# Kernel tuning notes

Hardware: AMD Instinct MI355X
Metric: run time of the kernel (lower is better)

## Reference

```python
import jax, jax.numpy as jnp
import numpy as np

B_SZ, C, H, W = 64, 256, 28, 28
HEADS, HEAD_DIM = 4, 64
BLOCK, HALO = 4, 4
WIN = BLOCK + 2 * HALO  # 12
KCONV = 3


def _unfold(x, k, s, p):
    # torch F.unfold semantics; returns [b, c, oh, kh, ow, kw]
    b, c, h, w = x.shape
    xp = jnp.pad(x, ((0, 0), (0, 0), (p, p), (p, p)))
    oh = (h + 2 * p - k) // s + 1
    ow = (w + 2 * p - k) // s + 1
    ih = jnp.arange(oh)[:, None] * s + jnp.arange(k)[None, :]
    iw = jnp.arange(ow)[:, None] * s + jnp.arange(k)[None, :]
    pt = xp[:, :, ih]            # [b,c,oh,kh,Wp]
    pt = pt[:, :, :, :, iw]      # [b,c,oh,kh,ow,kw]
    return pt


def _rel_to_abs(x):
    # x: [b, l, 2r-1] -> [b, l, r] via shift trick
    b, l, m = x.shape
    r = (m + 1) // 2
    x = jnp.pad(x, ((0, 0), (0, 0), (0, 1))).reshape(b, l * (m + 1))
    x = jnp.pad(x, ((0, 0), (0, m - l))).reshape(b, l + 1, m)
    return x[:, :l, -r:]


def _relative_logits_1d(q, rel_k):
    # q: [b, x, y, d], rel_k: [2r-1, d] -> [b, x, i(=r), y, j(=r)]
    b, h, w, _ = q.shape
    r = (rel_k.shape[0] + 1) // 2
    logits = jnp.einsum('bxyd,rd->bxyr', q, rel_k)
    logits = _rel_to_abs(logits.reshape(b * h, w, 2 * r - 1)).reshape(b, h, w, r)
    return jnp.broadcast_to(logits[:, :, None], (b, h, r, w, r))


def _rel_pos_emb(q, rel_height, rel_width):
    # q: [B, block^2, d]
    B, n, d = q.shape
    qb = q.reshape(B, BLOCK, BLOCK, d)
    lw = _relative_logits_1d(qb, rel_width)                 # [B,x,i,y,j]
    lw = lw.transpose(0, 1, 3, 2, 4).reshape(B, n, -1)      # b (x y) (i j)
    qh = qb.transpose(0, 2, 1, 3)
    lh = _relative_logits_1d(qh, rel_height)                # [B,y,i,x,j]
    lh = lh.transpose(0, 3, 1, 4, 2).reshape(B, n, -1)      # b (y x) (j i)
    return lw + lh


def setup_inputs() -> dict:
    key = jax.random.key(0)
    ks = jax.random.split(key, 13)
    f = jnp.float32
    rel_scale = HEAD_DIM ** (-0.5)
    return {
        'x': jax.random.normal(ks[0], (B_SZ, C, H, W), dtype=f),
        'w1': jax.random.normal(ks[1], (C, C), dtype=f) * 0.05,
        'b1': jax.random.normal(ks[2], (C,), dtype=f) * 0.05,
        'w2': jax.random.normal(ks[3], (C, C), dtype=f) * 0.05,
        'b2': jax.random.normal(ks[4], (C,), dtype=f) * 0.05,
        'w3': jax.random.normal(ks[5], (C, C), dtype=f) * 0.05,
        'b3': jax.random.normal(ks[6], (C,), dtype=f) * 0.05,
        'fc_w': jax.random.normal(ks[7], (KCONV * KCONV, 3 * HEADS), dtype=f) * 0.1,
        'dep_w': jax.random.normal(ks[8], (C, KCONV * KCONV, KCONV, KCONV), dtype=f) * 0.05,
        'rel_height': jax.random.normal(ks[9], (2 * WIN - 1, HEAD_DIM), dtype=f) * rel_scale,
        'rel_width': jax.random.normal(ks[10], (2 * WIN - 1, HEAD_DIM), dtype=f) * rel_scale,
        'rate1': jax.random.normal(ks[11], (1,), dtype=f),
        'rate2': jax.random.normal(ks[12], (1,), dtype=f),
    }


def reference(x, w1, b1, w2, b2, w3, b3, fc_w, dep_w, rel_height, rel_width, rate1, rate2):
    b = x.shape[0]
    scaling = HEAD_DIM ** (-0.5)
    q = jnp.einsum('bchw,oc->bohw', x, w1) + b1[None, :, None, None]
    k = jnp.einsum('bchw,oc->bohw', x, w2) + b2[None, :, None, None]
    v = jnp.einsum('bchw,oc->bohw', x, w3) + b3[None, :, None, None]
    c = q.shape[1]
    nb = H // BLOCK          # 7 blocks per side
    nwin = nb * nb           # 49 windows
    n_q = BLOCK * BLOCK      # 16 queries per window
    n_k = WIN * WIN          # 144 keys per window (with halo)

    # block queries: b c (h p1) (w p2) -> (b h w) (p1 p2) c
    q_att = q.reshape(b, c, nb, BLOCK, nb, BLOCK).transpose(0, 2, 4, 3, 5, 1).reshape(b * nwin, n_q, c)
    kp = _unfold(k, WIN, BLOCK, HALO).transpose(0, 2, 4, 3, 5, 1).reshape(b * nwin, n_k, c)
    vp = _unfold(v, WIN, BLOCK, HALO).transpose(0, 2, 4, 3, 5, 1).reshape(b * nwin, n_k, c)

    def split_heads(t):
        Bn, n, _ = t.shape
        return t.reshape(Bn, n, HEADS, HEAD_DIM).transpose(0, 2, 1, 3).reshape(Bn * HEADS, n, HEAD_DIM)

    q1 = split_heads(q_att) * scaling
    k1 = split_heads(kp)
    v1 = split_heads(vp)

    sim = jnp.einsum('bid,bjd->bij', q1, k1)
    sim = sim + _rel_pos_emb(q1, rel_height, rel_width)

    # NOTE: faithfully reproduces original (valid positions get -max, padded get 0)
    ones = jnp.ones((1, 1, H, W), x.dtype)
    valid = _unfold(ones, WIN, BLOCK, HALO).transpose(0, 2, 4, 3, 5, 1).reshape(nwin, n_k) > 0
    big_neg = -jnp.finfo(sim.dtype).max
    sim = sim.reshape(b, nwin, HEADS, n_q, n_k)
    sim = jnp.where(valid[None, :, None, None, :], big_neg, sim)
    attn = jax.nn.softmax(sim, axis=-1).reshape(b * nwin * HEADS, n_q, n_k)

    out = jnp.einsum('bij,bjd->bid', attn, v1)
    out = out.reshape(b * nwin, HEADS, n_q, HEAD_DIM).transpose(0, 2, 1, 3)  # merge heads
    out = out.reshape(b, nb, nb, BLOCK, BLOCK, c)
    out_att = out.transpose(0, 5, 1, 3, 2, 4).reshape(b, c, H, W)

    # conv branch: fc over concatenated per-head q,k,v, then depthwise-grouped conv
    f_all = jnp.concatenate([
        q.reshape(b, HEADS, HEAD_DIM, H * W),
        k.reshape(b, HEADS, HEAD_DIM, H * W),
        v.reshape(b, HEADS, HEAD_DIM, H * W)], axis=1)        # [b, 3*heads, hd, HW]
    f_all = jnp.einsum('bcmn,oc->bomn', f_all, fc_w)          # [b, 9, hd, HW]
    f_conv = f_all.transpose(0, 2, 1, 3).reshape(b, HEAD_DIM * KCONV * KCONV, H, W)
    out_conv = jax.lax.conv_general_dilated(
        f_conv, dep_w, window_strides=(1, 1), padding=((1, 1), (1, 1)),
        dimension_numbers=('NCHW', 'OIHW', 'NCHW'), feature_group_count=HEAD_DIM)

    return rate1[0] * out_att + rate2[0] * out_conv
```

## Files before the change

kernel.cpp:

```cpp
#include <hip/hip_runtime.h>
#include <hip/hip_bf16.h>

typedef __hip_bfloat16 bf16;
typedef unsigned int uint;
typedef unsigned short ushort;

using frag8 = __attribute__((ext_vector_type(8))) short;
using f32x4 = __attribute__((ext_vector_type(4))) float;

#define HWH 784
#define PPITCH 30
#define PPLANE 900
#define PBLK 10800

__global__ __launch_bounds__(256) void fold_w2(const float* __restrict__ fc_w,
                                               const float* __restrict__ dep_w,
                                               const float* __restrict__ b1,
                                               const float* __restrict__ b2,
                                               const float* __restrict__ b3,
                                               float* __restrict__ W2,
                                               float* __restrict__ biascat) {
    int idx = blockIdx.x * 256 + threadIdx.x;
    if (idx < 768) {
        const float* bs = idx < 256 ? b1 : (idx < 512 ? b2 : b3);
        biascat[idx] = bs[idx & 255];
    }
    if (idx >= 256 * 108) return;
    int oc  = idx / 108;
    int r   = idx % 108;
    int c12 = r / 9;
    int k9  = r % 9;
    float s = 0.f;
#pragma unroll
    for (int o = 0; o < 9; ++o)
        s += fc_w[o * 12 + c12] * dep_w[oc * 81 + o * 9 + k9];
    W2[idx] = s;
}

__global__ __launch_bounds__(256) void wprep(const float* __restrict__ w1,
                                             const float* __restrict__ w2,
                                             const float* __restrict__ w3,
                                             bf16* __restrict__ wbf) {
    int row = blockIdx.x, tid = threadIdx.x;
    const float* src = row < 256 ? w1 : (row < 512 ? w2 : w3);
    wbf[row * 256 + tid] = __float2bfloat16(src[(row & 255) * 256 + tid]);
}

__global__ __launch_bounds__(256) void xpose(const float* __restrict__ x,
                                             bf16* __restrict__ xT) {
    __shared__ float t[32][33];
    const int n0 = blockIdx.x * 32, c0 = blockIdx.y * 32, b = blockIdx.z;
    const int tid = threadIdx.x;
    const float* xb = x + (size_t)b * (256 * HWH);
#pragma unroll
    for (int e = tid; e < 1024; e += 256) {
        int r = e >> 5, col = e & 31;
        int n = n0 + col;
        t[r][col] = (n < HWH) ? xb[(size_t)(c0 + r) * HWH + n] : 0.f;
    }
    __syncthreads();
#pragma unroll
    for (int e = tid; e < 512; e += 256) {
        int r = e >> 4, cp = (e & 15) * 2;
        int n = n0 + r;
        if (n < HWH) {
            __hip_bfloat162 h;
            h.x = __float2bfloat16(t[cp][r]);
            h.y = __float2bfloat16(t[cp + 1][r]);
            *reinterpret_cast<__hip_bfloat162*>(
                &xT[((size_t)b * HWH + n) * 256 + c0 + cp]) = h;
        }
    }
}

__device__ inline void load_lds16(const bf16* g, short* lds) {
    __builtin_amdgcn_global_load_lds(
        (const __attribute__((address_space(1))) void*)g,
        (__attribute__((address_space(3))) void*)lds, 16, 0, 0);
}

__global__ __launch_bounds__(256) void gemm_mfma(const bf16* __restrict__ wbf,
                                                 const float* __restrict__ biascat,
                                                 const bf16* __restrict__ xT,
                                                 bf16* __restrict__ perm) {
    __shared__ short lds[8192];

    const int tid  = threadIdx.x;
    const int wave = tid >> 6, lane = tid & 63;

    const int s  = blockIdx.x;
    const int X  = s & 7, j = s >> 3;
    const int G  = X * 56 + j / 6;
    const int mt = j % 6;
    const int nt = G % 7;
    const int b  = G / 7;

    const int m0   = mt * 128;
    const int n0   = nt * 128;
    const int mw   = wave & 1, nw = wave >> 1;
    const int lrow = lane & 15, lkc = lane >> 4;

    f32x4 acc[4][4] = {};
    const bf16* xb = xT + (size_t)b * (HWH * 256);

    for (int k0 = 0; k0 < 256; k0 += 32) {
#pragma unroll
        for (int i = 0; i < 2; ++i) {
            const int jb = 2 * wave + i;
            const bf16* ga = wbf + (size_t)(m0 + 16 * jb + lrow) * 256 + k0 + lkc * 8;
            load_lds16(ga, &lds[jb * 512]);
            int n = n0 + 16 * jb + lrow;
            if (n > HWH - 1) n = HWH - 1;
            const bf16* gb = xb + (size_t)n * 256 + k0 + lkc * 8;
            load_lds16(gb, &lds[4096 + jb * 512]);
        }
        __syncthreads();

        frag8 af[4], bf_[4];
#pragma unroll
        for (int i = 0; i < 4; ++i)
            af[i] = *reinterpret_cast<const frag8*>(&lds[(4 * mw + i) * 512 + lane * 8]);
#pragma unroll
        for (int j2 = 0; j2 < 4; ++j2)
            bf_[j2] = *reinterpret_cast<const frag8*>(&lds[4096 + (4 * nw + j2) * 512 + lane * 8]);
#pragma unroll
        for (int i = 0; i < 4; ++i)
#pragma unroll
            for (int j2 = 0; j2 < 4; ++j2)
                acc[i][j2] = __builtin_amdgcn_mfma_f32_16x16x32_bf16(
                    af[i], bf_[j2], acc[i][j2], 0, 0, 0);
        __syncthreads();
    }

#pragma unroll
    for (int i = 0; i < 4; ++i) {
        const int rowb = m0 + mw * 64 + i * 16 + lkc * 4;
        bf16* base[4]; float bias4[4];
#pragma unroll
        for (int r = 0; r < 4; ++r) {
            const int m = rowb + r;
            const int sec = m >> 8, ch = m & 255;
            base[r] = perm + ((size_t)b * 64 + (ch & 63)) * PBLK
                           + (size_t)(sec * 4 + (ch >> 6)) * PPLANE;
            bias4[r] = biascat[m];
        }
#pragma unroll
        for (int j2 = 0; j2 < 4; ++j2) {
            const int col = n0 + nw * 64 + j2 * 16 + lrow;
            if (col < HWH) {
                const int pos = col + 2 * (col / 28) + 31;
#pragma unroll
                for (int r = 0; r < 4; ++r)
                    base[r][pos] = __float2bfloat16(acc[i][j2][r] + bias4[r]);
            }
        }
    }
}

__global__ __launch_bounds__(256) void attmean(const bf16* __restrict__ perm,
                                               const float* __restrict__ rate1,
                                               float* __restrict__ attm) {
    const int b = blockIdx.y, cg = blockIdx.x;
    const int wave = threadIdx.x >> 6, lane = threadIdx.x & 63;
    const int c = cg * 4 + wave;
    const bf16* vp = perm + ((size_t)(b * 64 + (c & 63)) * 12 + 8 + (c >> 6)) * (size_t)PPLANE;

    float cs[5] = {0.f, 0.f, 0.f, 0.f, 0.f};
    if (lane < 28) {
#pragma unroll
        for (int y = 0; y < 28; ++y) {
            float v = __bfloat162float(vp[(y + 1) * PPITCH + lane + 1]);
#pragma unroll
            for (int wi = 0; wi < 5; ++wi)
                if (y >= 4 * wi && y <= 4 * wi + 11) cs[wi] += v;
        }
    }
    const float r1s = rate1[0] * (1.0f / 144.0f);
#pragma unroll
    for (int wi = 0; wi < 5; ++wi) {
        float p = cs[wi];
#pragma unroll
        for (int d = 1; d < 32; d <<= 1) {
            float t = __shfl_up(p, d);
            if (lane >= d) p += t;
        }
        float hi = __shfl(p, 4 * lane + 11);
        float lo = __shfl(p, 4 * lane - 1);
        if (lane < 5) {
            float w = hi - (lane ? lo : 0.f);
            attm[((size_t)b * 256 + c) * 25 + wi * 5 + lane] = w * r1s;
        }
    }
}

__global__ __launch_bounds__(256) void out_fused5(
    const bf16* __restrict__ perm, const float* __restrict__ W2,
    const float* __restrict__ attm, const float* __restrict__ rate2,
    float* __restrict__ out) {
    __shared__ __align__(16) short planes[12 * PPLANE];
    __shared__ float w2s[4][12][12];
    __shared__ float attbs[4][25];

    const int g = blockIdx.x, b = blockIdx.y, tid = threadIdx.x;

    const uint4* src = (const uint4*)(perm + (size_t)(b * 64 + g) * PBLK);
#pragma unroll
    for (int it = 0; it < 6; ++it) {
        int e = tid + it * 256;
        if (e < 1350) ((uint4*)planes)[e] = src[e];
    }
    for (int e = tid; e < 576; e += 256) {
        int oc = e / 144, rem = e % 144, cc = rem / 12, k = rem % 12;
        w2s[oc][cc][k] = (k < 9) ? W2[(4 * g + oc) * 108 + cc * 9 + k] : 0.f;
    }
    if (tid < 100)
        attbs[tid / 25][tid % 25] =
            attm[((size_t)b * 256 + 4 * g + tid / 25) * 25 + tid % 25];
    __syncthreads();

    for (int e = tid; e < 1392; e += 256) {
        int c12 = e / 116, u = e % 116, idx;
        if (u < 30)      idx = u;
        else if (u < 60) idx = 870 + (u - 30);
        else { int v = u - 60; idx = ((v >> 1) + 1) * PPITCH + (v & 1) * 29; }
        planes[c12 * PPLANE + idx] = 0;
    }
    __syncthreads();

    float acc[4][4] = {};
    const int y = tid % 28, xs = tid / 28, x0 = xs * 4;
    if (tid < 196) {
#pragma unroll 1
        for (int c = 0; c < 12; ++c) {
            float rr[3][6];
#pragma unroll
            for (int dy = 0; dy < 3; ++dy) {
                const uint* row = (const uint*)&planes[c * PPLANE + (y + dy) * PPITCH + x0];
#pragma unroll
                for (int jp = 0; jp < 3; ++jp) {
                    uint w = row[jp];
                    float2 f = __bfloat1622float2(*(const __hip_bfloat162*)&w);
                    rr[dy][2 * jp]     = f.x;
                    rr[dy][2 * jp + 1] = f.y;
                }
            }
#pragma unroll
            for (int oc = 0; oc < 4; ++oc) {
                const float4* wr = reinterpret_cast<const float4*>(&w2s[oc][c][0]);
                float4 wa = wr[0], wb = wr[1], wc = wr[2];
                const float wk[9] = {wa.x, wa.y, wa.z, wa.w, wb.x, wb.y, wb.z, wb.w, wc.x};
#pragma unroll
                for (int ky = 0; ky < 3; ++ky)
#pragma unroll
                    for (int kx = 0; kx < 3; ++kx) {
                        float wv = wk[ky * 3 + kx];
#pragma unroll
                        for (int px = 0; px < 4; ++px)
                            acc[oc][px] += wv * rr[ky][px + kx];
                    }
            }
        }

        const float r2 = rate2[0];
        const int wi = (y >> 2) - 1, wj = xs - 1;
        const bool inter = (wi >= 0) & (wi < 5) & (wj >= 0) & (wj < 5);
#pragma unroll
        for (int oc = 0; oc < 4; ++oc) {
            float av = inter ? attbs[oc][wi * 5 + wj] : 0.f;
            float4 o;
            o.x = av + r2 * acc[oc][0];
            o.y = av + r2 * acc[oc][1];
            o.z = av + r2 * acc[oc][2];
            o.w = av + r2 * acc[oc][3];
            *reinterpret_cast<float4*>(
                &out[((size_t)(b * 256 + 4 * g + oc)) * HWH + y * 28 + x0]) = o;
        }
    }
}

extern "C" void kernel_launch(void* const* d_in, const int* in_sizes, int n_in,
                              void* d_out, int out_size, void* d_ws, size_t ws_size,
                              hipStream_t stream) {
    const float* x     = (const float*)d_in[0];
    const float* w1    = (const float*)d_in[1];
    const float* b1    = (const float*)d_in[2];
    const float* w2    = (const float*)d_in[3];
    const float* b2    = (const float*)d_in[4];
    const float* w3    = (const float*)d_in[5];
    const float* b3    = (const float*)d_in[6];
    const float* fc_w  = (const float*)d_in[7];
    const float* dep_w = (const float*)d_in[8];
    const float* rate1 = (const float*)d_in[11];
    const float* rate2 = (const float*)d_in[12];
    float* out = (float*)d_out;

    char* wsb = (char*)d_ws;
    bf16*  perm    = (bf16*)wsb;
    bf16*  xT      = (bf16*)(wsb + 88473600);
    float* attm    = (float*)(wsb + 88473600);
    bf16*  wbf     = (bf16*)(wsb + 114163712);
    float* W2      = (float*)(wsb + 114556928);
    float* biascat = (float*)(wsb + 114667520);

    fold_w2   <<<dim3(108),        dim3(256), 0, stream>>>(fc_w, dep_w, b1, b2, b3, W2, biascat);
    wprep     <<<dim3(768),        dim3(256), 0, stream>>>(w1, w2, w3, wbf);
    xpose     <<<dim3(25, 8, 64),  dim3(256), 0, stream>>>(x, xT);
    gemm_mfma <<<dim3(2688),       dim3(256), 0, stream>>>(wbf, biascat, xT, perm);
    attmean   <<<dim3(64, 64),     dim3(256), 0, stream>>>(perm, rate1, attm);
    out_fused5<<<dim3(64, 64),     dim3(256), 0, stream>>>(perm, W2, attm, rate2, out);
}
```

Before: 249.7 us.

## Swap MFMA operands and widen padded plane pitch for vectorized GEMM epilogue stores

Swaps the A/B operands of the MFMA so each lane holds four consecutive spatial positions for one channel instead of four channels for one position. The padded plane layout is changed to pitch 34, with data starting at column offset 2, so those four values can be written as two aligned bf16x2 stores rather than four scattered 2-byte stores. The consumers (attmean and out_fused5) are updated for the new pitch, border zeroing and offsets. This costs about 13% more workspace and LDS traffic per plane, plus one extra row load in the conv loop.

```diff
diff --git a/kernel.cpp b/kernel.cpp
--- a/kernel.cpp
+++ b/kernel.cpp
@@ -9,9 +9,9 @@
 using f32x4 = __attribute__((ext_vector_type(4))) float;
 
 #define HWH 784
-#define PPITCH 30
-#define PPLANE 900
-#define PBLK 10800
+#define PPITCH 34
+#define PPLANE 1020
+#define PBLK 12240
 
 __global__ __launch_bounds__(256) void fold_w2(const float* __restrict__ fc_w,
                                                const float* __restrict__ dep_w,
@@ -128,30 +128,29 @@
 #pragma unroll
             for (int j2 = 0; j2 < 4; ++j2)
                 acc[i][j2] = __builtin_amdgcn_mfma_f32_16x16x32_bf16(
-                    af[i], bf_[j2], acc[i][j2], 0, 0, 0);
+                    bf_[j2], af[i], acc[i][j2], 0, 0, 0);
         __syncthreads();
     }
 
 #pragma unroll
     for (int i = 0; i < 4; ++i) {
-        const int rowb = m0 + mw * 64 + i * 16 + lkc * 4;
-        bf16* base[4]; float bias4[4];
-#pragma unroll
-        for (int r = 0; r < 4; ++r) {
-            const int m = rowb + r;
-            const int sec = m >> 8, ch = m & 255;
-            base[r] = perm + ((size_t)b * 64 + (ch & 63)) * PBLK
-                           + (size_t)(sec * 4 + (ch >> 6)) * PPLANE;
-            bias4[r] = biascat[m];
-        }
+        const int m = m0 + mw * 64 + i * 16 + lrow;
+        const int sec = m >> 8, ch = m & 255;
+        bf16* const base = perm + ((size_t)b * 64 + (ch & 63)) * PBLK
+                         + (size_t)(sec * 4 + (ch >> 6)) * PPLANE;
+        const float bias = biascat[m];
 #pragma unroll
         for (int j2 = 0; j2 < 4; ++j2) {
-            const int col = n0 + nw * 64 + j2 * 16 + lrow;
-            if (col < HWH) {
-                const int pos = col + 2 * (col / 28) + 31;
-#pragma unroll
-                for (int r = 0; r < 4; ++r)
-                    base[r][pos] = __float2bfloat16(acc[i][j2][r] + bias4[r]);
+            const int n = n0 + nw * 64 + j2 * 16 + lkc * 4;
+            if (n < HWH) {
+                const int pos = n + 6 * (n / 28) + 36;
+                __hip_bfloat162 lo, hi;
+                lo.x = __float2bfloat16(acc[i][j2][0] + bias);
+                lo.y = __float2bfloat16(acc[i][j2][1] + bias);
+                hi.x = __float2bfloat16(acc[i][j2][2] + bias);
+                hi.y = __float2bfloat16(acc[i][j2][3] + bias);
+                *reinterpret_cast<__hip_bfloat162*>(&base[pos])     = lo;
+                *reinterpret_cast<__hip_bfloat162*>(&base[pos + 2]) = hi;
             }
         }
     }
@@ -169,7 +168,7 @@
     if (lane < 28) {
 #pragma unroll
         for (int y = 0; y < 28; ++y) {
-            float v = __bfloat162float(vp[(y + 1) * PPITCH + lane + 1]);
+            float v = __bfloat162float(vp[(y + 1) * PPITCH + lane + 2]);
 #pragma unroll
             for (int wi = 0; wi < 5; ++wi)
                 if (y >= 4 * wi && y <= 4 * wi + 11) cs[wi] += v;
@@ -207,7 +206,7 @@
 #pragma unroll
     for (int it = 0; it < 6; ++it) {
         int e = tid + it * 256;
-        if (e < 1350) ((uint4*)planes)[e] = src[e];
+        if (e < 1530) ((uint4*)planes)[e] = src[e];
     }
     for (int e = tid; e < 576; e += 256) {
         int oc = e / 144, rem = e % 144, cc = rem / 12, k = rem % 12;
@@ -220,9 +219,9 @@
 
     for (int e = tid; e < 1392; e += 256) {
         int c12 = e / 116, u = e % 116, idx;
-        if (u < 30)      idx = u;
-        else if (u < 60) idx = 870 + (u - 30);
-        else { int v = u - 60; idx = ((v >> 1) + 1) * PPITCH + (v & 1) * 29; }
+        if (u < 30)      idx = u + 1;
+        else if (u < 60) idx = 29 * PPITCH + (u - 30) + 1;
+        else { int v = u - 60; idx = ((v >> 1) + 1) * PPITCH + ((v & 1) ? 30 : 1); }
         planes[c12 * PPLANE + idx] = 0;
     }
     __syncthreads();
@@ -232,12 +231,12 @@
     if (tid < 196) {
 #pragma unroll 1
         for (int c = 0; c < 12; ++c) {
-            float rr[3][6];
+            float rr[3][8];
 #pragma unroll
             for (int dy = 0; dy < 3; ++dy) {
                 const uint* row = (const uint*)&planes[c * PPLANE + (y + dy) * PPITCH + x0];
 #pragma unroll
-                for (int jp = 0; jp < 3; ++jp) {
+                for (int jp = 0; jp < 4; ++jp) {
                     uint w = row[jp];
                     float2 f = __bfloat1622float2(*(const __hip_bfloat162*)&w);
                     rr[dy][2 * jp]     = f.x;
@@ -256,7 +255,7 @@
                         float wv = wk[ky * 3 + kx];
 #pragma unroll
                         for (int px = 0; px < 4; ++px)
-                            acc[oc][px] += wv * rr[ky][px + kx];
+                            acc[oc][px] += wv * rr[ky][px + kx + 1];
                     }
             }
         }
@@ -296,11 +295,11 @@
 
     char* wsb = (char*)d_ws;
     bf16*  perm    = (bf16*)wsb;
-    bf16*  xT      = (bf16*)(wsb + 88473600);
-    float* attm    = (float*)(wsb + 88473600);
-    bf16*  wbf     = (bf16*)(wsb + 114163712);
-    float* W2      = (float*)(wsb + 114556928);
-    float* biascat = (float*)(wsb + 114667520);
+    bf16*  xT      = (bf16*)(wsb + 100270080);
+    float* attm    = (float*)(wsb + 100270080);
+    bf16*  wbf     = (bf16*)(wsb + 125960192);
+    float* W2      = (float*)(wsb + 126353408);
+    float* biascat = (float*)(wsb + 126464000);
 
     fold_w2   <<<dim3(108),        dim3(256), 0, stream>>>(fc_w, dep_w, b1, b2, b3, W2, biascat);
     wprep     <<<dim3(768),        dim3(256), 0, stream>>>(w1, w2, w3, wbf);
```

Result: slower. 260.2 us (+4.2%).
